# Optimization experiments

Hardware: AMD Instinct MI355X
Metric: run time of the kernel (lower is better)

## Reference

```python
import jax, jax.numpy as jnp
import numpy as np

R = 0.9  # compression ratio from init_kwargs


def _dct_matrix(N):
    """Orthonormal DCT-II matrix C of shape [N, N].
    (C @ v) along the last axis equals dct(v, norm='ortho').
    Its transpose is the orthonormal DCT-III (inverse)."""
    n = jnp.arange(N, dtype=jnp.float32)
    k = n[:, None]
    C = jnp.cos(jnp.pi * (2.0 * n[None, :] + 1.0) * k / (2.0 * N))
    s = jnp.full((N,), jnp.sqrt(2.0 / N), dtype=jnp.float32).at[0].set(jnp.sqrt(1.0 / N))
    return s[:, None] * C


def setup_inputs() -> dict:
    key = jax.random.key(0)
    # hidden states [B, T, D]
    x = jax.random.normal(key, (64, 1024, 768), dtype=jnp.float32)
    return {"x": x}


def reference(x):
    """CompressedModel.compress_hidden_state with compress_method='dct' and
    use_compressed_hidden_state=True:
      1) DCT-II (ortho) along the token axis T
      2) keep the first k = ceil(r*T) coefficients
      3) inverse DCT (ortho, size k) to reconstruct a shorter sequence
    Returns (x_reconstructed [B,k,D], x_dct [B,k,D]) matching dc_transform."""
    B, T, D = x.shape
    k = int(np.ceil(R * T))  # static under jit
    C_T = _dct_matrix(T)          # [T, T]
    # DCT along tokens, truncate to low-frequency k coeffs
    x_dct = jnp.einsum('kt,btd->bkd', C_T, x)[:, :k, :]  # [B, k, D]
    # inverse DCT of size k (DCT-III ortho = transpose of DCT-II ortho)
    C_k = _dct_matrix(k)          # [k, k]
    x_rec = jnp.einsum('mn,bmd->bnd', C_k, x_dct)         # [B, k, D]
    return x_rec, x_dct
```

## Files before the change

kernel.cpp:

```cpp
#include <hip/hip_runtime.h>
#include <hip/hip_bf16.h>

typedef __attribute__((ext_vector_type(8))) short short8;
typedef __attribute__((ext_vector_type(4))) float f32x4;

#define T_LEN   1024
#define KKEEP   922
#define DDIM    768
#define NBATCH  64


__global__ void gen_C1(__hip_bfloat16* __restrict__ C1) {
    int idx = blockIdx.x * 256 + threadIdx.x;
    if (idx >= 1024 * 1024) return;
    int kk = idx >> 10;
    int t  = idx & 1023;
    float val = 0.0f;
    if (kk < KKEEP) {
        float a1 = 3.14159265358979323846f * (2.0f * (float)t + 1.0f);
        float a2 = a1 * (float)kk;
        float a3 = a2 / 2048.0f;
        float s  = (kk == 0) ? sqrtf(1.0f / 1024.0f) : sqrtf(2.0f / 1024.0f);
        val = s * cosf(a3);
    }
    C1[idx] = __float2bfloat16(val);
}

__global__ void gen_C2T(__hip_bfloat16* __restrict__ A2) {
    int idx = blockIdx.x * 256 + threadIdx.x;
    if (idx >= 1024 * 928) return;
    int n = idx / 928;
    int m = idx - n * 928;
    float val = 0.0f;
    if (n < KKEEP && m < KKEEP) {
        float a1 = 3.14159265358979323846f * (2.0f * (float)n + 1.0f);
        float a2 = a1 * (float)m;
        float a3 = a2 / 1844.0f;
        float s  = (m == 0) ? sqrtf(1.0f / 922.0f) : sqrtf(2.0f / 922.0f);
        val = s * cosf(a3);
    }
    A2[idx] = __float2bfloat16(val);
}

__global__ __launch_bounds__(256)
void transpose_cvt(const float* __restrict__ in, __hip_bfloat16* __restrict__ out,
                   int R, int C, int Rp)
{
    __shared__ float tile[64][65];
    const int r0 = blockIdx.x * 64, c0 = blockIdx.y * 64, z = blockIdx.z;
    const float* inz = in + (size_t)z * R * C;
    __hip_bfloat16* outz = out + (size_t)z * C * Rp;
    const int tid = threadIdx.x;
    const int lr = tid >> 4, lc4 = (tid & 15) * 4;
    #pragma unroll
    for (int i = 0; i < 4; ++i) {
        int row = i * 16 + lr;
        int gr  = r0 + row;
        float4 v = make_float4(0.f, 0.f, 0.f, 0.f);
        if (gr < R) v = *(const float4*)(inz + (size_t)gr * C + c0 + lc4);
        tile[row][lc4 + 0] = v.x; tile[row][lc4 + 1] = v.y;
        tile[row][lc4 + 2] = v.z; tile[row][lc4 + 3] = v.w;
    }
    __syncthreads();
    const int orow = tid >> 2, seg = tid & 3;
    const int rB = r0 + seg * 16;
    if (rB < Rp) {
        alignas(16) __hip_bfloat16 tmp[16];
        #pragma unroll
        for (int j = 0; j < 16; ++j)
            tmp[j] = __float2bfloat16(tile[seg * 16 + j][orow]);
        uint4* dst = (uint4*)(outz + (size_t)(c0 + orow) * Rp + rB);
        dst[0] = ((const uint4*)tmp)[0];
        dst[1] = ((const uint4*)tmp)[1];
    }
}

__global__ __launch_bounds__(256)
void gemm_bf16(const __hip_bfloat16* __restrict__ A, int lda,
               const __hip_bfloat16* __restrict__ B, int ldb, long long bStride,
               float* __restrict__ C, long long cStride, int ksteps)
{
    __shared__ __hip_bfloat16 As[2][128 * 32];
    __shared__ __hip_bfloat16 Bs[2][128 * 32];

    const int tid   = threadIdx.x;
    const int mBase = blockIdx.y * 128;
    const int nBase = blockIdx.x * 128;
    const __hip_bfloat16* __restrict__ Bb = B + (long long)blockIdx.z * bStride;
    float* __restrict__ Cb = C + (long long)blockIdx.z * cStride;

    auto stage = [&](int buf, int k0) {
        #pragma unroll
        for (int h = 0; h < 2; ++h) {
            int c = h * 256 + tid;
            int row = c >> 2, q = c & 3;
            const __hip_bfloat16* ga = A + (size_t)(mBase + row) * lda + k0 + q * 8;
            __builtin_amdgcn_global_load_lds(
                (const __attribute__((address_space(1))) void*)ga,
                (__attribute__((address_space(3))) void*)(&As[buf][c * 8]), 16, 0, 0);
            const __hip_bfloat16* gb = Bb + (size_t)(nBase + row) * ldb + k0 + q * 8;
            __builtin_amdgcn_global_load_lds(
                (const __attribute__((address_space(1))) void*)gb,
                (__attribute__((address_space(3))) void*)(&Bs[buf][c * 8]), 16, 0, 0);
        }
    };

    const int lane = tid & 63;
    const int wid  = tid >> 6;
    const int wm   = (wid >> 1) * 64;
    const int wn   = (wid & 1) * 64;
    const int lr   = lane & 15;
    const int g8   = (lane >> 4) * 8;

    f32x4 acc[4][4] = {};

    stage(0, 0);
    for (int s = 0; s < ksteps; ++s) {
        int buf = s & 1;
        __syncthreads();
        if (s + 1 < ksteps) stage(buf ^ 1, (s + 1) * 32);
        short8 af[4], bfr[4];
        #pragma unroll
        for (int m = 0; m < 4; ++m)
            af[m] = *(const short8*)&As[buf][(wm + m * 16 + lr) * 32 + g8];
        #pragma unroll
        for (int n = 0; n < 4; ++n)
            bfr[n] = *(const short8*)&Bs[buf][(wn + n * 16 + lr) * 32 + g8];
        #pragma unroll
        for (int m = 0; m < 4; ++m)
            #pragma unroll
            for (int n = 0; n < 4; ++n)
                acc[m][n] = __builtin_amdgcn_mfma_f32_16x16x32_bf16(af[m], bfr[n], acc[m][n], 0, 0, 0);
    }

    #pragma unroll
    for (int m = 0; m < 4; ++m) {
        int row0 = mBase + wm + m * 16 + (lane >> 4) * 4;
        #pragma unroll
        for (int n = 0; n < 4; ++n) {
            int col = nBase + wn + n * 16 + lr;
            #pragma unroll
            for (int i = 0; i < 4; ++i) {
                int row = row0 + i;
                if (row < KKEEP)
                    Cb[(size_t)row * DDIM + col] = acc[m][n][i];
            }
        }
    }
}

#define BK 32
#define LDSK 40
__global__ __launch_bounds__(256)
void gemm_dct(const __hip_bfloat16* __restrict__ A, int lda, int ksteps,
              const float* __restrict__ B, int bRows, long long bStride,
              float* __restrict__ C, long long cStride)
{
    __shared__ __hip_bfloat16 As[2][128 * LDSK];
    __shared__ __hip_bfloat16 Bs[2][128 * LDSK];
    const int tid   = threadIdx.x;
    const int mBase = blockIdx.y * 128;
    const int nBase = blockIdx.x * 128;
    const float* __restrict__ Bb = B + (long long)blockIdx.z * bStride;
    float* __restrict__       Cb = C + (long long)blockIdx.z * cStride;

    auto stageA = [&](int buf, int k0) {
        int r = tid >> 1, half = tid & 1;
        const uint4* src = (const uint4*)(A + (size_t)(mBase + r) * lda + k0 + half * 16);
        uint4 v0 = src[0], v1 = src[1];
        uint4* dst = (uint4*)&As[buf][r * LDSK + half * 16];
        dst[0] = v0; dst[1] = v1;
    };
    auto stageB = [&](int buf, int k0) {
        #pragma unroll
        for (int p = 0; p < 4; ++p) {
            int idx = p * 256 + tid;
            int k   = idx & 31;
            int n4  = (idx >> 5) * 4;
            int gk  = k0 + k;
            float4 v = make_float4(0.f, 0.f, 0.f, 0.f);
            if (gk < bRows) v = *(const float4*)(Bb + (size_t)gk * DDIM + nBase + n4);
            __hip_bfloat16* d = &Bs[buf][n4 * LDSK + k];
            d[0 * LDSK] = __float2bfloat16(v.x);
            d[1 * LDSK] = __float2bfloat16(v.y);
            d[2 * LDSK] = __float2bfloat16(v.z);
            d[3 * LDSK] = __float2bfloat16(v.w);
        }
    };

    const int lane = tid & 63;
    const int wid  = tid >> 6;
    const int wm   = (wid >> 1) * 64;
    const int wn   = (wid & 1) * 64;
    const int lr   = lane & 15;
    const int g8   = (lane >> 4) * 8;
    f32x4 acc[4][4] = {};

    stageA(0, 0);
    stageB(0, 0);
    __syncthreads();
    for (int s = 0; s < ksteps; ++s) {
        int buf = s & 1;
        if (s + 1 < ksteps) {
            stageA(buf ^ 1, (s + 1) * BK);
            stageB(buf ^ 1, (s + 1) * BK);
        }
        short8 af[4], bfr[4];
        #pragma unroll
        for (int m = 0; m < 4; ++m)
            af[m] = *(const short8*)&As[buf][(wm + m * 16 + lr) * LDSK + g8];
        #pragma unroll
        for (int n = 0; n < 4; ++n)
            bfr[n] = *(const short8*)&Bs[buf][(wn + n * 16 + lr) * LDSK + g8];
        #pragma unroll
        for (int m = 0; m < 4; ++m)
            #pragma unroll
            for (int n = 0; n < 4; ++n)
                acc[m][n] = __builtin_amdgcn_mfma_f32_16x16x32_bf16(af[m], bfr[n], acc[m][n], 0, 0, 0);
        __syncthreads();
    }
    #pragma unroll
    for (int m = 0; m < 4; ++m) {
        int row0 = mBase + wm + m * 16 + (lane >> 4) * 4;
        #pragma unroll
        for (int n = 0; n < 4; ++n) {
            int col = nBase + wn + n * 16 + lr;
            #pragma unroll
            for (int i = 0; i < 4; ++i) {
                int row = row0 + i;
                if (row < KKEEP)
                    Cb[(size_t)row * DDIM + col] = acc[m][n][i];
            }
        }
    }
}

extern "C" void kernel_launch(void* const* d_in, const int* in_sizes, int n_in,
                              void* d_out, int out_size, void* d_ws, size_t ws_size,
                              hipStream_t stream)
{
    const float* x = (const float*)d_in[0];
    float* out  = (float*)d_out;
    float* xrec = out;
    float* xdct = out + (size_t)NBATCH * KKEEP * DDIM;

    const size_t SZ_C1  = 1024ull * 1024;
    const size_t SZ_A2  = 1024ull * 928;
    const size_t SZ_XDT = 64ull * 768 * 928;

    __hip_bfloat16* C1 = (__hip_bfloat16*)d_ws;
    __hip_bfloat16* A2 = C1 + SZ_C1;
    const bool bigws = ws_size >= (SZ_C1 + SZ_A2 + SZ_XDT) * 2;
    __hip_bfloat16* xdT = A2 + SZ_A2;

    __hip_bfloat16* xT = (__hip_bfloat16*)xrec;

    gen_C1<<<(1024 * 1024 + 255) / 256, 256, 0, stream>>>(C1);
    gen_C2T<<<(1024 * 928 + 255) / 256, 256, 0, stream>>>(A2);

    transpose_cvt<<<dim3(16, 12, NBATCH), 256, 0, stream>>>(x, xT, 1024, DDIM, 1024);

    dim3 grid(DDIM / 128, 1024 / 128, NBATCH);

    gemm_bf16<<<grid, 256, 0, stream>>>(C1, 1024, xT, 1024,
                                        (long long)DDIM * 1024,
                                        xdct, (long long)KKEEP * DDIM, 32);

    if (bigws) {
        transpose_cvt<<<dim3(15, 12, NBATCH), 256, 0, stream>>>(xdct, xdT, KKEEP, DDIM, 928);
        gemm_bf16<<<grid, 256, 0, stream>>>(A2, 928, xdT, 928,
                                            (long long)DDIM * 928,
                                            xrec, (long long)KKEEP * DDIM, 29);
    } else {
        gemm_dct<<<grid, 256, 0, stream>>>(A2, 928, 29,
                                           xdct, KKEEP, (long long)KKEEP * DDIM,
                                           xrec, (long long)KKEEP * DDIM);
    }
}
```

Measured before the change: 791.0 us.

## Fuse transposed bf16 xdct write into first GEMM epilogue and remap block order

The first DCT GEMM now also writes a transposed bf16 copy of its output directly from the accumulators. This removes the separate transpose_cvt kernel that re-read the fp32 xdct. The block index is also remapped so that consecutive workgroups spread across XCDs in a chunked order, with the aim of better cache locality. The transposed writes are strided 8-byte stores, which may coalesce poorly.

```diff
diff --git a/kernel.cpp b/kernel.cpp
--- a/kernel.cpp
+++ b/kernel.cpp
@@ -75,19 +75,29 @@
     }
 }
 
+template <bool WRT>
 __global__ __launch_bounds__(256)
 void gemm_bf16(const __hip_bfloat16* __restrict__ A, int lda,
                const __hip_bfloat16* __restrict__ B, int ldb, long long bStride,
-               float* __restrict__ C, long long cStride, int ksteps)
+               float* __restrict__ C, long long cStride, int ksteps,
+               __hip_bfloat16* __restrict__ DT, int ldt, long long dtStride)
 {
     __shared__ __hip_bfloat16 As[2][128 * 32];
     __shared__ __hip_bfloat16 Bs[2][128 * 32];
 
+    const int orig = blockIdx.x + 6 * (blockIdx.y + 8 * blockIdx.z);
+    const int w    = (orig & 7) * 384 + (orig >> 3);
+    const int bx   = w % 6;
+    const int tmp  = w / 6;
+    const int by   = tmp & 7;
+    const int bz   = tmp >> 3;
+
     const int tid   = threadIdx.x;
-    const int mBase = blockIdx.y * 128;
-    const int nBase = blockIdx.x * 128;
-    const __hip_bfloat16* __restrict__ Bb = B + (long long)blockIdx.z * bStride;
-    float* __restrict__ Cb = C + (long long)blockIdx.z * cStride;
+    const int mBase = by * 128;
+    const int nBase = bx * 128;
+    const __hip_bfloat16* __restrict__ Bb = B + (long long)bz * bStride;
+    float* __restrict__ Cb = C + (long long)bz * cStride;
+    __hip_bfloat16* __restrict__ DTb = WRT ? (DT + (long long)bz * dtStride) : nullptr;
 
     auto stage = [&](int buf, int k0) {
         #pragma unroll
@@ -144,6 +154,12 @@
                 int row = row0 + i;
                 if (row < KKEEP)
                     Cb[(size_t)row * DDIM + col] = acc[m][n][i];
+            }
+            if (WRT && row0 < 928) {
+                union { ushort4 u; __hip_bfloat16 h[4]; } t;
+                #pragma unroll
+                for (int i = 0; i < 4; ++i) t.h[i] = __float2bfloat16(acc[m][n][i]);
+                *(ushort4*)(DTb + (size_t)col * ldt + row0) = t.u;
             }
         }
     }
@@ -262,16 +278,20 @@
 
     dim3 grid(DDIM / 128, 1024 / 128, NBATCH);
 
-    gemm_bf16<<<grid, 256, 0, stream>>>(C1, 1024, xT, 1024,
-                                        (long long)DDIM * 1024,
-                                        xdct, (long long)KKEEP * DDIM, 32);
-
     if (bigws) {
-        transpose_cvt<<<dim3(15, 12, NBATCH), 256, 0, stream>>>(xdct, xdT, KKEEP, DDIM, 928);
-        gemm_bf16<<<grid, 256, 0, stream>>>(A2, 928, xdT, 928,
-                                            (long long)DDIM * 928,
-                                            xrec, (long long)KKEEP * DDIM, 29);
+        gemm_bf16<true><<<grid, 256, 0, stream>>>(C1, 1024, xT, 1024,
+                                                  (long long)DDIM * 1024,
+                                                  xdct, (long long)KKEEP * DDIM, 32,
+                                                  xdT, 928, (long long)DDIM * 928);
+        gemm_bf16<false><<<grid, 256, 0, stream>>>(A2, 928, xdT, 928,
+                                                   (long long)DDIM * 928,
+                                                   xrec, (long long)KKEEP * DDIM, 29,
+                                                   nullptr, 0, 0);
     } else {
+        gemm_bf16<false><<<grid, 256, 0, stream>>>(C1, 1024, xT, 1024,
+                                                   (long long)DDIM * 1024,
+                                                   xdct, (long long)KKEEP * DDIM, 32,
+                                                   nullptr, 0, 0);
         gemm_dct<<<grid, 256, 0, stream>>>(A2, 928, 29,
                                            xdct, KKEEP, (long long)KKEEP * DDIM,
                                            xrec, (long long)KKEEP * DDIM);
```

New measurement: 782.2 us. About the same (-1.1%).
